# Optimization experiments

Hardware: AMD Instinct MI355X
Metric: run time of the kernel (lower is better)

## Reference

```python
import jax, jax.numpy as jnp
import numpy as np

B = 4096
V = 50257
K = 64
LABEL_SMOOTHING = 0.1


def setup_inputs() -> dict:
    key = jax.random.key(0)
    k1, k2 = jax.random.split(key)
    inp = jax.random.normal(k1, (B, V), dtype=jnp.float32)
    target = jax.random.randint(k2, (B,), 0, V, dtype=jnp.int64)
    return {"input": inp, "target": target}


def reference(input, target):
    rows = jnp.arange(input.shape[0])
    # gather the true-class logit: (B, 1)
    truth = input[rows, target][:, None]
    # mask the true class to -inf so top-k selects k hardest negatives
    masked = input.at[rows, target].set(-jnp.inf)
    topk_vals = jax.lax.top_k(masked, K)[0]          # (B, K)
    selected = jnp.concatenate([truth, topk_vals], axis=-1)  # (B, K+1)
    # cross-entropy with target class 0 and label smoothing (torch semantics:
    # loss = (1-eps)*nll + eps * mean_c(-log p_c))
    logp = jax.nn.log_softmax(selected, axis=-1)
    nll = -logp[:, 0]
    smooth = -jnp.mean(logp, axis=-1)
    per_ex = (1.0 - LABEL_SMOOTHING) * nll + LABEL_SMOOTHING * smooth
    return jnp.mean(per_ex)
```

## Files before the change

### kernel.cpp

```cpp
#include <hip/hip_runtime.h>
#include <math.h>
#include <stdint.h>

#define BROWS 4096
#define VCOLS 50257
#define KTOP  64
#define CAP   2048
#define CHECK_AT 1024
#define NREG 32

__device__ __forceinline__ unsigned f2key(float f) {
    unsigned u = __float_as_uint(f);
    return u ^ ((unsigned)((int)u >> 31) | 0x80000000u);
}
__device__ __forceinline__ float key2f(unsigned k) {
    unsigned u = (k & 0x80000000u) ? (k ^ 0x80000000u) : ~k;
    return __uint_as_float(u);
}

__device__ __forceinline__ int wave_sum_i(int c) {
    #pragma unroll
    for (int d = 1; d < 64; d <<= 1) c += __shfl_xor(c, d);
    return c;
}

__device__ __forceinline__ void load_keys(const float* s_buf, unsigned cnt, int lane, unsigned* key) {
    #pragma unroll
    for (int j = 0; j < NREG / 4; ++j) {
        const float4 v = ((const float4*)s_buf)[j * 64 + lane];
        const int base = (j * 64 + lane) * 4;
        key[4*j+0] = (base + 0 < (int)cnt) ? f2key(v.x) : 0u;
        key[4*j+1] = (base + 1 < (int)cnt) ? f2key(v.y) : 0u;
        key[4*j+2] = (base + 2 < (int)cnt) ? f2key(v.z) : 0u;
        key[4*j+3] = (base + 3 < (int)cnt) ? f2key(v.w) : 0u;
    }
}

__device__ __forceinline__ void wave_compact(float* s_buf, unsigned& cnt, float& thr, int lane) {
    __builtin_amdgcn_wave_barrier();
    unsigned key[NREG];
    load_keys(s_buf, cnt, lane, key);
    unsigned kmx = 0u;
    #pragma unroll
    for (int j = 0; j < NREG; ++j) kmx = max(kmx, key[j]);
    #pragma unroll
    for (int d = 1; d < 64; d <<= 1) kmx = max(kmx, (unsigned)__shfl_xor((int)kmx, d));

    unsigned lo = f2key(thr);
    unsigned hi = kmx + 1u;
    for (int it = 0; it < 12; ++it) {
        if (hi - lo <= 1u) break;
        const unsigned mid = lo + ((hi - lo) >> 1);
        int c = 0;
        #pragma unroll
        for (int j = 0; j < NREG; ++j) c += (key[j] >= mid) ? 1 : 0;
        c = wave_sum_i(c);
        if (c >= KTOP) lo = mid; else hi = mid;
    }
    int cl = 0; unsigned sm = 0u;
    #pragma unroll
    for (int j = 0; j < NREG; ++j) { const bool s = key[j] >= lo; sm |= (unsigned)s << j; cl += s ? 1 : 0; }
    int incl = cl;
    #pragma unroll
    for (int d = 1; d < 64; d <<= 1) { const int t = __shfl_up(incl, d); if (lane >= d) incl += t; }
    int pos = incl - cl;
    __builtin_amdgcn_wave_barrier();
    #pragma unroll
    for (int j = 0; j < NREG; ++j) if ((sm >> j) & 1u) s_buf[pos++] = key2f(key[j]);
    cnt = (unsigned)__shfl(incl, 63);
    thr = key2f(lo);
    __builtin_amdgcn_wave_barrier();
}

__device__ __forceinline__ float wave_final(const float* s_buf, unsigned cnt, float thr, float tv, int lane) {
    __builtin_amdgcn_wave_barrier();
    unsigned key[NREG];
    load_keys(s_buf, cnt, lane, key);
    unsigned kmx = 0u;
    #pragma unroll
    for (int j = 0; j < NREG; ++j) kmx = max(kmx, key[j]);
    #pragma unroll
    for (int d = 1; d < 64; d <<= 1) kmx = max(kmx, (unsigned)__shfl_xor((int)kmx, d));

    unsigned lo = f2key(thr);
    unsigned hi = kmx + 1u;
    while (hi - lo > 1u) {
        const unsigned mid = lo + ((hi - lo) >> 1);
        int c = 0;
        #pragma unroll
        for (int j = 0; j < NREG; ++j) c += (key[j] >= mid) ? 1 : 0;
        c = wave_sum_i(c);
        if (c >= KTOP) lo = mid; else hi = mid;
    }
    const float vmax = key2f(kmx);
    const float m = fmaxf(vmax, tv);
    float se = 0.f, sv = 0.f; int cg = 0;
    #pragma unroll
    for (int j = 0; j < NREG; ++j) {
        if (key[j] > lo) { const float v = key2f(key[j]); se += __expf(v - m); sv += v; ++cg; }
    }
    #pragma unroll
    for (int d = 1; d < 64; d <<= 1) {
        se += __shfl_xor(se, d); sv += __shfl_xor(sv, d); cg += __shfl_xor(cg, d);
    }
    const float v64 = key2f(lo);
    const int nb = KTOP - cg;
    se += (float)nb * __expf(v64 - m);
    sv += (float)nb * v64;
    se += __expf(tv - m);
    const float lse = m + __logf(se);
    return lse - 0.9f * tv - 0.1f * ((sv + tv) * (1.0f / 65.0f));
}

__device__ __forceinline__ void ins1(float v, int gi, int tgt, float thr,
                                     float* s_buf, unsigned& cnt, unsigned long long lt) {
    const bool p = (v > thr) && (gi != tgt);
    const unsigned long long mk = __ballot(p ? 1 : 0);
    if (mk) {
        if (p) {
            const unsigned pos = cnt + (unsigned)__popcll(mk & lt);
            if (pos < CAP) s_buf[pos] = v;
        }
        cnt += (unsigned)__popcll(mk);
    }
}
__device__ __forceinline__ void ins4(const float4 q, int gb, int tgt, float thr,
                                     float* s_buf, unsigned& cnt, unsigned long long lt) {
    ins1(q.x, gb + 0, tgt, thr, s_buf, cnt, lt);
    ins1(q.y, gb + 1, tgt, thr, s_buf, cnt, lt);
    ins1(q.z, gb + 2, tgt, thr, s_buf, cnt, lt);
    ins1(q.w, gb + 3, tgt, thr, s_buf, cnt, lt);
}

__global__ __launch_bounds__(64) void topk_ce_kernel(
        const float* __restrict__ input, const int* __restrict__ target,
        float* __restrict__ per_ex, float* __restrict__ out_atomic) {
    __shared__ float s_buf[CAP];
    const int row  = blockIdx.x;
    const int lane = threadIdx.x;
    const float* __restrict__ rowp = input + (size_t)row * (size_t)VCOLS;
    const int tgt = target[row];
    const unsigned long long lt = (1ull << lane) - 1ull;

    unsigned cnt = 0u;
    float thr = -INFINITY;

    const int pad = (int)((4u - ((((uintptr_t)rowp) >> 2) & 3u)) & 3u);
    {
        const float v = (lane < pad) ? rowp[lane] : 0.f;
        const bool p = (lane < pad) && (lane != tgt);
        const unsigned long long mk = __ballot(p ? 1 : 0);
        if (p) s_buf[cnt + __popcll(mk & lt)] = v;
        cnt += (unsigned)__popcll(mk);
    }

    const int nvec  = (VCOLS - pad) >> 2;
    const int ntail = (VCOLS - pad) & 3;
    const float4* __restrict__ vp = (const float4*)(rowp + pad);
    const int ntf = nvec >> 8;

    for (int t = 0; t < ntf; ++t) {
        const int b0 = t * 256 + lane;
        const float4 a = vp[b0];
        const float4 b = vp[b0 + 64];
        const float4 c = vp[b0 + 128];
        const float4 d = vp[b0 + 192];
        const float mA = fmaxf(fmaxf(a.x, a.y), fmaxf(a.z, a.w));
        const float mB = fmaxf(fmaxf(b.x, b.y), fmaxf(b.z, b.w));
        const float mC = fmaxf(fmaxf(c.x, c.y), fmaxf(c.z, c.w));
        const float mD = fmaxf(fmaxf(d.x, d.y), fmaxf(d.z, d.w));
        const float m16 = fmaxf(fmaxf(mA, mB), fmaxf(mC, mD));
        if (__ballot((m16 > thr) ? 1 : 0)) {
            ins4(a, pad + 4 * b0,         tgt, thr, s_buf, cnt, lt);
            ins4(b, pad + 4 * (b0 + 64),  tgt, thr, s_buf, cnt, lt);
            ins4(c, pad + 4 * (b0 + 128), tgt, thr, s_buf, cnt, lt);
            ins4(d, pad + 4 * (b0 + 192), tgt, thr, s_buf, cnt, lt);
        }
        if (cnt > CHECK_AT) wave_compact(s_buf, cnt, thr, lane);
    }

    for (int k0 = ntf * 256; k0 < nvec; k0 += 64) {
        const int idx = k0 + lane;
        float4 a;
        if (idx < nvec) a = vp[idx];
        else { a.x = a.y = a.z = a.w = -INFINITY; }
        const float mA = fmaxf(fmaxf(a.x, a.y), fmaxf(a.z, a.w));
        if (__ballot((mA > thr) ? 1 : 0))
            ins4(a, pad + 4 * idx, tgt, thr, s_buf, cnt, lt);
        if (cnt > CHECK_AT) wave_compact(s_buf, cnt, thr, lane);
    }

    {
        const int idx = pad + 4 * nvec + lane;
        const float v = (lane < ntail) ? rowp[idx] : 0.f;
        const bool p = (lane < ntail) && (v > thr) && (idx != tgt);
        const unsigned long long mk = __ballot(p ? 1 : 0);
        if (p) s_buf[cnt + __popcll(mk & lt)] = v;
        cnt += (unsigned)__popcll(mk);
    }

    const float tv = rowp[tgt];
    const float pe = wave_final(s_buf, cnt, thr, tv, lane);
    if (lane == 0) {
        if (per_ex) per_ex[row] = pe;
        else atomicAdd(out_atomic, pe * (1.0f / BROWS));
    }
}

__global__ __launch_bounds__(256) void reduce_mean_kernel(
        const float* __restrict__ per_ex, float* __restrict__ out) {
    __shared__ float s[256];
    const int tid = threadIdx.x;
    float acc = 0.0f;
    for (int i = tid; i < BROWS; i += 256) acc += per_ex[i];
    s[tid] = acc;
    __syncthreads();
    for (int w = 128; w > 0; w >>= 1) {
        if (tid < w) s[tid] += s[tid + w];
        __syncthreads();
    }
    if (tid == 0) out[0] = s[0] * (1.0f / BROWS);
}

extern "C" void kernel_launch(void* const* d_in, const int* in_sizes, int n_in,
                              void* d_out, int out_size, void* d_ws, size_t ws_size,
                              hipStream_t stream) {
    const float* input  = (const float*)d_in[0];
    const int*   target = (const int*)d_in[1];
    float* out = (float*)d_out;

    if (ws_size >= BROWS * sizeof(float)) {
        float* per_ex = (float*)d_ws;
        topk_ce_kernel<<<BROWS, 64, 0, stream>>>(input, target, per_ex, nullptr);
        reduce_mean_kernel<<<1, 256, 0, stream>>>(per_ex, out);
    } else {
        hipMemsetAsync(d_out, 0, sizeof(float), stream);
        topk_ce_kernel<<<BROWS, 64, 0, stream>>>(input, target, nullptr, out);
    }
}
```

Baseline: 179.5 us.

## Split each row across two waves with software-pipelined loads and merged top-64

Each row is now handled by a 128-thread block. Each of the two waves scans half the vocabulary into its own LDS candidate buffer. Tile loads are double-buffered in registers so the next 4-float4 tile is in flight while the current one is filtered. Each wave trims its candidates to a local top-64 in shared memory, and wave 0 merges the 128 values with a bisection search before computing the loss. This aims to halve per-row serial latency and raise memory-level parallelism, at the cost of more registers, double the LDS per block, and a block barrier.

```diff
diff --git a/kernel.cpp b/kernel.cpp
--- a/kernel.cpp
+++ b/kernel.cpp
@@ -5,6 +5,7 @@
 #define BROWS 4096
 #define VCOLS 50257
 #define KTOP  64
+#define NTH   128
 #define CAP   2048
 #define CHECK_AT 1024
 #define NREG 32
@@ -72,7 +73,8 @@
     __builtin_amdgcn_wave_barrier();
 }
 
-__device__ __forceinline__ float wave_final(const float* s_buf, unsigned cnt, float thr, float tv, int lane) {
+__device__ __forceinline__ void wave_trim64(const float* s_buf, unsigned cnt, float thr,
+                                            int lane, float* out64) {
     __builtin_amdgcn_wave_barrier();
     unsigned key[NREG];
     load_keys(s_buf, cnt, lane, key);
@@ -92,24 +94,18 @@
         c = wave_sum_i(c);
         if (c >= KTOP) lo = mid; else hi = mid;
     }
-    const float vmax = key2f(kmx);
-    const float m = fmaxf(vmax, tv);
-    float se = 0.f, sv = 0.f; int cg = 0;
-    #pragma unroll
-    for (int j = 0; j < NREG; ++j) {
-        if (key[j] > lo) { const float v = key2f(key[j]); se += __expf(v - m); sv += v; ++cg; }
-    }
-    #pragma unroll
-    for (int d = 1; d < 64; d <<= 1) {
-        se += __shfl_xor(se, d); sv += __shfl_xor(sv, d); cg += __shfl_xor(cg, d);
-    }
+    int cl = 0; unsigned sm = 0u;
+    #pragma unroll
+    for (int j = 0; j < NREG; ++j) { const bool s = key[j] > lo; sm |= (unsigned)s << j; cl += s ? 1 : 0; }
+    int incl = cl;
+    #pragma unroll
+    for (int d = 1; d < 64; d <<= 1) { const int t = __shfl_up(incl, d); if (lane >= d) incl += t; }
+    int pos = incl - cl;
+    #pragma unroll
+    for (int j = 0; j < NREG; ++j) if ((sm >> j) & 1u) out64[pos++] = key2f(key[j]);
+    const int total = __shfl(incl, 63);
     const float v64 = key2f(lo);
-    const int nb = KTOP - cg;
-    se += (float)nb * __expf(v64 - m);
-    sv += (float)nb * v64;
-    se += __expf(tv - m);
-    const float lse = m + __logf(se);
-    return lse - 0.9f * tv - 0.1f * ((sv + tv) * (1.0f / 65.0f));
+    for (int i = total + lane; i < KTOP; i += 64) out64[i] = v64;
 }
 
 __device__ __forceinline__ void ins1(float v, int gi, int tgt, float thr,
@@ -132,12 +128,36 @@
     ins1(q.w, gb + 3, tgt, thr, s_buf, cnt, lt);
 }
 
-__global__ __launch_bounds__(64) void topk_ce_kernel(
+#define LOADT(A0,A1,A2,A3, tq) do { const int b_ = q0 + (tq)*256 + lane; \
+    A0 = vp[b_]; A1 = vp[b_+64]; A2 = vp[b_+128]; A3 = vp[b_+192]; } while (0)
+
+#define PROC(A0,A1,A2,A3, tq) do { \
+    const int bq_ = q0 + (tq)*256 + lane; \
+    const float mA_ = fmaxf(fmaxf(A0.x,A0.y), fmaxf(A0.z,A0.w)); \
+    const float mB_ = fmaxf(fmaxf(A1.x,A1.y), fmaxf(A1.z,A1.w)); \
+    const float mC_ = fmaxf(fmaxf(A2.x,A2.y), fmaxf(A2.z,A2.w)); \
+    const float mD_ = fmaxf(fmaxf(A3.x,A3.y), fmaxf(A3.z,A3.w)); \
+    const float m16_ = fmaxf(fmaxf(mA_,mB_), fmaxf(mC_,mD_)); \
+    if (__ballot((m16_ > thr) ? 1 : 0)) { \
+        ins4(A0, pad + 4*bq_,       tgt, thr, buf, cnt, lt); \
+        ins4(A1, pad + 4*(bq_+64),  tgt, thr, buf, cnt, lt); \
+        ins4(A2, pad + 4*(bq_+128), tgt, thr, buf, cnt, lt); \
+        ins4(A3, pad + 4*(bq_+192), tgt, thr, buf, cnt, lt); \
+    } \
+    if (cnt > CHECK_AT) wave_compact(buf, cnt, thr, lane); \
+} while (0)
+
+__global__ __launch_bounds__(NTH) void topk_ce_kernel(
         const float* __restrict__ input, const int* __restrict__ target,
         float* __restrict__ per_ex, float* __restrict__ out_atomic) {
-    __shared__ float s_buf[CAP];
+    __shared__ float s_buf[2][CAP];
+    __shared__ float s_top[2 * KTOP];
+
     const int row  = blockIdx.x;
-    const int lane = threadIdx.x;
+    const int tid  = threadIdx.x;
+    const int wid  = tid >> 6;
+    const int lane = tid & 63;
+    float* buf = s_buf[wid];
     const float* __restrict__ rowp = input + (size_t)row * (size_t)VCOLS;
     const int tgt = target[row];
     const unsigned long long lt = (1ull << lane) - 1ull;
@@ -146,64 +166,95 @@
     float thr = -INFINITY;
 
     const int pad = (int)((4u - ((((uintptr_t)rowp) >> 2) & 3u)) & 3u);
-    {
+    if (wid == 0) {
         const float v = (lane < pad) ? rowp[lane] : 0.f;
         const bool p = (lane < pad) && (lane != tgt);
         const unsigned long long mk = __ballot(p ? 1 : 0);
-        if (p) s_buf[cnt + __popcll(mk & lt)] = v;
+        if (p) buf[cnt + __popcll(mk & lt)] = v;
         cnt += (unsigned)__popcll(mk);
     }
 
     const int nvec  = (VCOLS - pad) >> 2;
     const int ntail = (VCOLS - pad) & 3;
     const float4* __restrict__ vp = (const float4*)(rowp + pad);
-    const int ntf = nvec >> 8;
-
-    for (int t = 0; t < ntf; ++t) {
-        const int b0 = t * 256 + lane;
-        const float4 a = vp[b0];
-        const float4 b = vp[b0 + 64];
-        const float4 c = vp[b0 + 128];
-        const float4 d = vp[b0 + 192];
-        const float mA = fmaxf(fmaxf(a.x, a.y), fmaxf(a.z, a.w));
-        const float mB = fmaxf(fmaxf(b.x, b.y), fmaxf(b.z, b.w));
-        const float mC = fmaxf(fmaxf(c.x, c.y), fmaxf(c.z, c.w));
-        const float mD = fmaxf(fmaxf(d.x, d.y), fmaxf(d.z, d.w));
-        const float m16 = fmaxf(fmaxf(mA, mB), fmaxf(mC, mD));
-        if (__ballot((m16 > thr) ? 1 : 0)) {
-            ins4(a, pad + 4 * b0,         tgt, thr, s_buf, cnt, lt);
-            ins4(b, pad + 4 * (b0 + 64),  tgt, thr, s_buf, cnt, lt);
-            ins4(c, pad + 4 * (b0 + 128), tgt, thr, s_buf, cnt, lt);
-            ins4(d, pad + 4 * (b0 + 192), tgt, thr, s_buf, cnt, lt);
-        }
-        if (cnt > CHECK_AT) wave_compact(s_buf, cnt, thr, lane);
-    }
-
-    for (int k0 = ntf * 256; k0 < nvec; k0 += 64) {
-        const int idx = k0 + lane;
+
+    const int nv0 = ((nvec + 256) >> 9) << 8;
+    const int q0 = wid ? nv0 : 0;
+    const int q1 = wid ? nvec : nv0;
+    const int ntf = (q1 - q0) >> 8;
+
+    float4 a0, a1, a2, a3, c0, c1, c2, c3;
+    int t = 0;
+    if (ntf > 0) LOADT(a0, a1, a2, a3, 0);
+    for (; t + 2 <= ntf; t += 2) {
+        LOADT(c0, c1, c2, c3, t + 1);
+        PROC(a0, a1, a2, a3, t);
+        if (t + 2 < ntf) LOADT(a0, a1, a2, a3, t + 2);
+        PROC(c0, c1, c2, c3, t + 1);
+    }
+    if (t < ntf) PROC(a0, a1, a2, a3, t);
+
+    for (int k0i = q0 + ntf * 256; k0i < q1; k0i += 64) {
+        const int idx = k0i + lane;
         float4 a;
-        if (idx < nvec) a = vp[idx];
+        if (idx < q1) a = vp[idx];
         else { a.x = a.y = a.z = a.w = -INFINITY; }
         const float mA = fmaxf(fmaxf(a.x, a.y), fmaxf(a.z, a.w));
-        if (__ballot((mA > thr) ? 1 : 0))
-            ins4(a, pad + 4 * idx, tgt, thr, s_buf, cnt, lt);
-        if (cnt > CHECK_AT) wave_compact(s_buf, cnt, thr, lane);
-    }
-
-    {
+        if (__ballot((mA > thr) ? 1 : 0)) ins4(a, pad + 4 * idx, tgt, thr, buf, cnt, lt);
+        if (cnt > CHECK_AT) wave_compact(buf, cnt, thr, lane);
+    }
+
+    if (wid == 1) {
         const int idx = pad + 4 * nvec + lane;
         const float v = (lane < ntail) ? rowp[idx] : 0.f;
         const bool p = (lane < ntail) && (v > thr) && (idx != tgt);
         const unsigned long long mk = __ballot(p ? 1 : 0);
-        if (p) s_buf[cnt + __popcll(mk & lt)] = v;
+        if (p) {
+            const unsigned pos = cnt + (unsigned)__popcll(mk & lt);
+            if (pos < CAP) buf[pos] = v;
+        }
         cnt += (unsigned)__popcll(mk);
     }
 
-    const float tv = rowp[tgt];
-    const float pe = wave_final(s_buf, cnt, thr, tv, lane);
-    if (lane == 0) {
-        if (per_ex) per_ex[row] = pe;
-        else atomicAdd(out_atomic, pe * (1.0f / BROWS));
+    wave_trim64(buf, cnt, thr, lane, s_top + wid * KTOP);
+    __syncthreads();
+
+    if (wid == 0) {
+        const float tv = rowp[tgt];
+        unsigned k0 = f2key(s_top[lane]);
+        unsigned k1 = f2key(s_top[64 + lane]);
+        unsigned kmx = max(k0, k1), kmn = min(k0, k1);
+        #pragma unroll
+        for (int d = 1; d < 64; d <<= 1) {
+            kmx = max(kmx, (unsigned)__shfl_xor((int)kmx, d));
+            kmn = min(kmn, (unsigned)__shfl_xor((int)kmn, d));
+        }
+        unsigned lo = kmn, hi = kmx + 1u;
+        while (hi - lo > 1u) {
+            const unsigned mid = lo + ((hi - lo) >> 1);
+            int c = ((k0 >= mid) ? 1 : 0) + ((k1 >= mid) ? 1 : 0);
+            c = wave_sum_i(c);
+            if (c >= KTOP) lo = mid; else hi = mid;
+        }
+        const float v64 = key2f(lo);
+        const float m = fmaxf(key2f(kmx), tv);
+        float se = 0.f, sv = 0.f; int cg = 0;
+        if (k0 > lo) { const float v = key2f(k0); se += __expf(v - m); sv += v; ++cg; }
+        if (k1 > lo) { const float v = key2f(k1); se += __expf(v - m); sv += v; ++cg; }
+        #pragma unroll
+        for (int d = 1; d < 64; d <<= 1) {
+            se += __shfl_xor(se, d); sv += __shfl_xor(sv, d); cg += __shfl_xor(cg, d);
+        }
+        const int nb = KTOP - cg;
+        se += (float)nb * __expf(v64 - m);
+        sv += (float)nb * v64;
+        se += __expf(tv - m);
+        const float lse = m + __logf(se);
+        const float pe = lse - 0.9f * tv - 0.1f * ((sv + tv) * (1.0f / 65.0f));
+        if (lane == 0) {
+            if (per_ex) per_ex[row] = pe;
+            else atomicAdd(out_atomic, pe * (1.0f / BROWS));
+        }
     }
 }
 
@@ -231,10 +282,10 @@
 
     if (ws_size >= BROWS * sizeof(float)) {
         float* per_ex = (float*)d_ws;
-        topk_ce_kernel<<<BROWS, 64, 0, stream>>>(input, target, per_ex, nullptr);
+        topk_ce_kernel<<<BROWS, NTH, 0, stream>>>(input, target, per_ex, nullptr);
         reduce_mean_kernel<<<1, 256, 0, stream>>>(per_ex, out);
     } else {
         hipMemsetAsync(d_out, 0, sizeof(float), stream);
-        topk_ce_kernel<<<BROWS, 64, 0, stream>>>(input, target, nullptr, out);
-    }
-}
+        topk_ce_kernel<<<BROWS, NTH, 0, stream>>>(input, target, nullptr, out);
+    }
+}
```

New measurement: 248.4 us. 38.4% more time.

## Software-pipeline row tile loads and outline compaction into noinline function

Applied to the files above, without the earlier changes.

The main scan loop is double-buffered: the next 256-float4 tile is loaded into registers while the current tile is filtered and inserted, so global-load latency overlaps the ballot/insert work. The compaction routine is made noinline and returns the count and threshold packed in one value, which keeps the hot loop's register footprint small enough for the extra buffers. The target logit load is hoisted to the kernel start, and the tail insert gains a capacity bound check. The cost is more live registers per lane and a function-call overhead on the rare compaction path.

```diff
diff --git a/kernel.cpp b/kernel.cpp
--- a/kernel.cpp
+++ b/kernel.cpp
@@ -36,7 +36,8 @@
     }
 }
 
-__device__ __forceinline__ void wave_compact(float* s_buf, unsigned& cnt, float& thr, int lane) {
+__device__ __attribute__((noinline)) unsigned long long
+wave_compact_f(float* s_buf, unsigned cnt, unsigned lo_in, int lane) {
     __builtin_amdgcn_wave_barrier();
     unsigned key[NREG];
     load_keys(s_buf, cnt, lane, key);
@@ -46,7 +47,7 @@
     #pragma unroll
     for (int d = 1; d < 64; d <<= 1) kmx = max(kmx, (unsigned)__shfl_xor((int)kmx, d));
 
-    unsigned lo = f2key(thr);
+    unsigned lo = lo_in;
     unsigned hi = kmx + 1u;
     for (int it = 0; it < 12; ++it) {
         if (hi - lo <= 1u) break;
@@ -67,9 +68,9 @@
     __builtin_amdgcn_wave_barrier();
     #pragma unroll
     for (int j = 0; j < NREG; ++j) if ((sm >> j) & 1u) s_buf[pos++] = key2f(key[j]);
-    cnt = (unsigned)__shfl(incl, 63);
-    thr = key2f(lo);
-    __builtin_amdgcn_wave_barrier();
+    const unsigned ncnt = (unsigned)__shfl(incl, 63);
+    __builtin_amdgcn_wave_barrier();
+    return ((unsigned long long)ncnt << 32) | (unsigned long long)lo;
 }
 
 __device__ __forceinline__ float wave_final(const float* s_buf, unsigned cnt, float thr, float tv, int lane) {
@@ -132,6 +133,28 @@
     ins1(q.w, gb + 3, tgt, thr, s_buf, cnt, lt);
 }
 
+#define LOADT(A0,A1,A2,A3, tq) do { const int b_ = (tq)*256 + lane; \
+    A0 = vp[b_]; A1 = vp[b_+64]; A2 = vp[b_+128]; A3 = vp[b_+192]; } while (0)
+
+#define PROC(A0,A1,A2,A3, tq) do { \
+    const int bq_ = (tq)*256 + lane; \
+    const float mA_ = fmaxf(fmaxf(A0.x,A0.y), fmaxf(A0.z,A0.w)); \
+    const float mB_ = fmaxf(fmaxf(A1.x,A1.y), fmaxf(A1.z,A1.w)); \
+    const float mC_ = fmaxf(fmaxf(A2.x,A2.y), fmaxf(A2.z,A2.w)); \
+    const float mD_ = fmaxf(fmaxf(A3.x,A3.y), fmaxf(A3.z,A3.w)); \
+    const float m16_ = fmaxf(fmaxf(mA_,mB_), fmaxf(mC_,mD_)); \
+    if (__ballot((m16_ > thr) ? 1 : 0)) { \
+        ins4(A0, pad + 4*bq_,       tgt, thr, s_buf, cnt, lt); \
+        ins4(A1, pad + 4*(bq_+64),  tgt, thr, s_buf, cnt, lt); \
+        ins4(A2, pad + 4*(bq_+128), tgt, thr, s_buf, cnt, lt); \
+        ins4(A3, pad + 4*(bq_+192), tgt, thr, s_buf, cnt, lt); \
+    } \
+    if (cnt > CHECK_AT) { \
+        const unsigned long long r_ = wave_compact_f(s_buf, cnt, f2key(thr), lane); \
+        cnt = (unsigned)(r_ >> 32); thr = key2f((unsigned)r_); \
+    } \
+} while (0)
+
 __global__ __launch_bounds__(64) void topk_ce_kernel(
         const float* __restrict__ input, const int* __restrict__ target,
         float* __restrict__ per_ex, float* __restrict__ out_atomic) {
@@ -140,6 +163,7 @@
     const int lane = threadIdx.x;
     const float* __restrict__ rowp = input + (size_t)row * (size_t)VCOLS;
     const int tgt = target[row];
+    const float tv = rowp[tgt];
     const unsigned long long lt = (1ull << lane) - 1ull;
 
     unsigned cnt = 0u;
@@ -159,25 +183,16 @@
     const float4* __restrict__ vp = (const float4*)(rowp + pad);
     const int ntf = nvec >> 8;
 
-    for (int t = 0; t < ntf; ++t) {
-        const int b0 = t * 256 + lane;
-        const float4 a = vp[b0];
-        const float4 b = vp[b0 + 64];
-        const float4 c = vp[b0 + 128];
-        const float4 d = vp[b0 + 192];
-        const float mA = fmaxf(fmaxf(a.x, a.y), fmaxf(a.z, a.w));
-        const float mB = fmaxf(fmaxf(b.x, b.y), fmaxf(b.z, b.w));
-        const float mC = fmaxf(fmaxf(c.x, c.y), fmaxf(c.z, c.w));
-        const float mD = fmaxf(fmaxf(d.x, d.y), fmaxf(d.z, d.w));
-        const float m16 = fmaxf(fmaxf(mA, mB), fmaxf(mC, mD));
-        if (__ballot((m16 > thr) ? 1 : 0)) {
-            ins4(a, pad + 4 * b0,         tgt, thr, s_buf, cnt, lt);
-            ins4(b, pad + 4 * (b0 + 64),  tgt, thr, s_buf, cnt, lt);
-            ins4(c, pad + 4 * (b0 + 128), tgt, thr, s_buf, cnt, lt);
-            ins4(d, pad + 4 * (b0 + 192), tgt, thr, s_buf, cnt, lt);
-        }
-        if (cnt > CHECK_AT) wave_compact(s_buf, cnt, thr, lane);
-    }
+    float4 a0, a1, a2, a3, b0, b1, b2, b3;
+    int t = 0;
+    if (ntf > 0) LOADT(a0, a1, a2, a3, 0);
+    for (; t + 2 <= ntf; t += 2) {
+        LOADT(b0, b1, b2, b3, t + 1);
+        PROC(a0, a1, a2, a3, t);
+        if (t + 2 < ntf) LOADT(a0, a1, a2, a3, t + 2);
+        PROC(b0, b1, b2, b3, t + 1);
+    }
+    if (t < ntf) PROC(a0, a1, a2, a3, t);
 
     for (int k0 = ntf * 256; k0 < nvec; k0 += 64) {
         const int idx = k0 + lane;
@@ -185,9 +200,11 @@
         if (idx < nvec) a = vp[idx];
         else { a.x = a.y = a.z = a.w = -INFINITY; }
         const float mA = fmaxf(fmaxf(a.x, a.y), fmaxf(a.z, a.w));
-        if (__ballot((mA > thr) ? 1 : 0))
-            ins4(a, pad + 4 * idx, tgt, thr, s_buf, cnt, lt);
-        if (cnt > CHECK_AT) wave_compact(s_buf, cnt, thr, lane);
+        if (__ballot((mA > thr) ? 1 : 0)) ins4(a, pad + 4 * idx, tgt, thr, s_buf, cnt, lt);
+        if (cnt > CHECK_AT) {
+            const unsigned long long r = wave_compact_f(s_buf, cnt, f2key(thr), lane);
+            cnt = (unsigned)(r >> 32); thr = key2f((unsigned)r);
+        }
     }
 
     {
@@ -195,11 +212,13 @@
         const float v = (lane < ntail) ? rowp[idx] : 0.f;
         const bool p = (lane < ntail) && (v > thr) && (idx != tgt);
         const unsigned long long mk = __ballot(p ? 1 : 0);
-        if (p) s_buf[cnt + __popcll(mk & lt)] = v;
+        if (p) {
+            const unsigned pos = cnt + (unsigned)__popcll(mk & lt);
+            if (pos < CAP) s_buf[pos] = v;
+        }
         cnt += (unsigned)__popcll(mk);
     }
 
-    const float tv = rowp[tgt];
     const float pe = wave_final(s_buf, cnt, thr, tv, lane);
     if (lane == 0) {
         if (per_ex) per_ex[row] = pe;
```

Result: slower. 184.0 us (+2.5%).
